# Optimization experiments

Hardware: AMD Instinct MI355X
Metric: run time of the kernel (lower is better)

## Reference

```python
import jax, jax.numpy as jnp
import numpy as np

B, L, D, H, NL = 4, 2048, 1024, 4, 2
HD = D // H
FF = 4 * D
EPS = 1e-5


def layernorm(x, g, b):
    mu = jnp.mean(x, axis=-1, keepdims=True)
    var = jnp.mean(jnp.square(x - mu), axis=-1, keepdims=True)
    return (x - mu) * jax.lax.rsqrt(var + EPS) * g + b


def setup_inputs() -> dict:
    key = jax.random.key(0)
    ks = jax.random.split(key, 8)
    std = 0.02
    return {
        "x": jax.random.normal(ks[0], (B, L, 3 * D), dtype=jnp.float32),
        "w3d": jax.random.normal(ks[1], (D, 3 * D), dtype=jnp.float32) * std,
        "b3d": jnp.zeros((D,), jnp.float32),
        "ln1_g": jnp.ones((NL, D), jnp.float32),
        "ln1_b": jnp.zeros((NL, D), jnp.float32),
        "wqkv": jax.random.normal(ks[2], (NL, 3 * D, D), dtype=jnp.float32) * std,
        "bqkv": jnp.zeros((NL, 3 * D), jnp.float32),
        "wproj": jax.random.normal(ks[3], (NL, D, D), dtype=jnp.float32) * std,
        "bproj": jnp.zeros((NL, D), jnp.float32),
        "ln2_g": jnp.ones((NL, D), jnp.float32),
        "ln2_b": jnp.zeros((NL, D), jnp.float32),
        "w1": jax.random.normal(ks[4], (NL, FF, D), dtype=jnp.float32) * std,
        "b1": jnp.zeros((NL, FF), jnp.float32),
        "w2": jax.random.normal(ks[5], (NL, D, FF), dtype=jnp.float32) * std,
        "b2": jnp.zeros((NL, D), jnp.float32),
        "lnf_g": jnp.ones((D,), jnp.float32),
        "lnf_b": jnp.zeros((D,), jnp.float32),
    }


def reference(x, w3d, b3d, ln1_g, ln1_b, wqkv, bqkv, wproj, bproj,
              ln2_g, ln2_b, w1, b1, w2, b2, lnf_g, lnf_b):
    h = jnp.einsum('bli,di->bld', x, w3d) + b3d
    scale = 1.0 / jnp.sqrt(jnp.float32(HD))
    for i in range(NL):
        # attention block
        res = h
        hn = layernorm(h, ln1_g[i], ln1_b[i])
        qkv = jnp.einsum('bld,ed->ble', hn, wqkv[i]) + bqkv[i]  # [B,L,3D]
        qkv = qkv.reshape(B, L, 3, H, HD)
        q, k, v = qkv[:, :, 0], qkv[:, :, 1], qkv[:, :, 2]  # [B,L,H,HD]
        attn = jnp.einsum('bqhd,bkhd->bhqk', q, k) * scale
        attn = jax.nn.softmax(attn, axis=-1)
        o = jnp.einsum('bhqk,bkhd->bqhd', attn, v).reshape(B, L, D)
        h = res + jnp.einsum('bld,ed->ble', o, wproj[i]) + bproj[i]
        # FFN block
        res = h
        hn = layernorm(h, ln2_g[i], ln2_b[i])
        f = jnp.einsum('bld,fd->blf', hn, w1[i]) + b1[i]
        f = jax.nn.gelu(f, approximate=False)  # torch nn.GELU default is exact
        h = res + jnp.einsum('blf,df->bld', f, w2[i]) + b2[i]
    return layernorm(h, lnf_g, lnf_b)
```

## Files before the change

### kernel.cpp

```cpp
#include <hip/hip_runtime.h>
#include <cstdint>
#include <cstddef>

#define BATCH   4
#define L_SEQ   2048
#define DMODEL  1024
#define NHEAD   4
#define HDIM    256
#define FFDIM   4096
#define MROWS   (BATCH * L_SEQ)
#define NLAYER  2

typedef __bf16 bf16_t;
typedef __bf16 bf16x8 __attribute__((ext_vector_type(8)));
typedef __bf16 bf16x4 __attribute__((ext_vector_type(4)));
typedef float  floatx4 __attribute__((ext_vector_type(4)));

__device__ __forceinline__ void async_cp16(const void* g, void* l) {
  auto gp = reinterpret_cast<__attribute__((address_space(1))) void*>(
      reinterpret_cast<uintptr_t>(g));
  auto lp = reinterpret_cast<__attribute__((address_space(3))) void*>(
      reinterpret_cast<uintptr_t>(l));
  __builtin_amdgcn_global_load_lds(gp, lp, 16, 0, 0);
}

__global__ __launch_bounds__(256)
void cvt_f32_bf16(const float* __restrict__ in, bf16_t* __restrict__ out, int n4) {
  int i = blockIdx.x * 256 + threadIdx.x;
  if (i >= n4) return;
  float4 v = ((const float4*)in)[i];
  bf16x4 ov = { (bf16_t)v.x, (bf16_t)v.y, (bf16_t)v.z, (bf16_t)v.w };
  ((bf16x4*)out)[i] = ov;
}

template<bool BF16OUT>
__global__ __launch_bounds__(256)
void ln_kernel(const float* __restrict__ x, const float* __restrict__ gw,
               const float* __restrict__ bw, void* __restrict__ outp) {
  const int row = blockIdx.x;
  const int tid = threadIdx.x;
  const float4 v = ((const float4*)(x + (size_t)row * DMODEL))[tid];
  float s  = v.x + v.y + v.z + v.w;
  float ss = v.x * v.x + v.y * v.y + v.z * v.z + v.w * v.w;
#pragma unroll
  for (int o = 32; o > 0; o >>= 1) {
    s  += __shfl_xor(s, o);
    ss += __shfl_xor(ss, o);
  }
  __shared__ float red0[4], red1[4];
  const int wv = tid >> 6;
  if ((tid & 63) == 0) { red0[wv] = s; red1[wv] = ss; }
  __syncthreads();
  s  = red0[0] + red0[1] + red0[2] + red0[3];
  ss = red1[0] + red1[1] + red1[2] + red1[3];
  const float mu  = s * (1.0f / DMODEL);
  const float var = ss * (1.0f / DMODEL) - mu * mu;
  const float rs  = rsqrtf(var + 1e-5f);
  const float4 g4 = ((const float4*)gw)[tid];
  const float4 b4 = ((const float4*)bw)[tid];
  const float o0 = (v.x - mu) * rs * g4.x + b4.x;
  const float o1 = (v.y - mu) * rs * g4.y + b4.y;
  const float o2 = (v.z - mu) * rs * g4.z + b4.z;
  const float o3 = (v.w - mu) * rs * g4.w + b4.w;
  if (BF16OUT) {
    bf16x4 ov = { (bf16_t)o0, (bf16_t)o1, (bf16_t)o2, (bf16_t)o3 };
    ((bf16x4*)outp)[(size_t)row * (DMODEL / 4) + tid] = ov;
  } else {
    float4 ov = { o0, o1, o2, o3 };
    ((float4*)outp)[(size_t)row * (DMODEL / 4) + tid] = ov;
  }
}

__global__ __launch_bounds__(256)
void softmax_kernel(bf16_t* __restrict__ S) {
  const size_t row = blockIdx.x;
  bf16_t* p = S + row * (size_t)L_SEQ + (size_t)threadIdx.x * 8;
  bf16x8 rv = *(const bf16x8*)p;
  float v[8];
  float mx = -1e30f;
#pragma unroll
  for (int j = 0; j < 8; ++j) { v[j] = (float)rv[j]; mx = fmaxf(mx, v[j]); }
#pragma unroll
  for (int o = 32; o > 0; o >>= 1) mx = fmaxf(mx, __shfl_xor(mx, o));
  __shared__ float sm[4], ssum[4];
  const int lane = threadIdx.x & 63, wv = threadIdx.x >> 6;
  if (lane == 0) sm[wv] = mx;
  __syncthreads();
  mx = fmaxf(fmaxf(sm[0], sm[1]), fmaxf(sm[2], sm[3]));
  float sum = 0.0f;
#pragma unroll
  for (int j = 0; j < 8; ++j) { v[j] = __expf(v[j] - mx); sum += v[j]; }
#pragma unroll
  for (int o = 32; o > 0; o >>= 1) sum += __shfl_xor(sum, o);
  if (lane == 0) ssum[wv] = sum;
  __syncthreads();
  sum = ssum[0] + ssum[1] + ssum[2] + ssum[3];
  const float inv = 1.0f / sum;
  bf16x8 ov;
#pragma unroll
  for (int j = 0; j < 8; ++j) ov[j] = (bf16_t)(v[j] * inv);
  *(bf16x8*)p = ov;
}

__global__ __launch_bounds__(256)
void transpose_v(const bf16_t* __restrict__ vt, bf16_t* __restrict__ vT) {
  __shared__ bf16_t tile[64][65];
  const int z = blockIdx.z, b = z >> 2, head = z & 3;
  const int l0 = blockIdx.x * 64, hd0 = blockIdx.y * 64;
  const int x = threadIdx.x & 63, y4 = threadIdx.x >> 6;
#pragma unroll
  for (int r = 0; r < 64; r += 4) {
    const int l = l0 + y4 + r;
    tile[y4 + r][x] =
        vt[((size_t)b * L_SEQ + l) * DMODEL + head * HDIM + hd0 + x];
  }
  __syncthreads();
#pragma unroll
  for (int r = 0; r < 64; r += 4) {
    const int hd = hd0 + y4 + r;
    vT[((size_t)z * HDIM + hd) * L_SEQ + l0 + x] = tile[x][y4 + r];
  }
}

struct EpiBiasF32 {
  float* C; const float* bias; int ldc;
  __device__ __forceinline__ void store(int, int m, int n, float v) const {
    C[(size_t)m * ldc + n] = v + bias[n];
  }
};
struct EpiResBiasF32 {
  float* C; const float* bias; int ldc;
  __device__ __forceinline__ void store(int, int m, int n, float v) const {
    const size_t idx = (size_t)m * ldc + n;
    C[idx] = C[idx] + v + bias[n];
  }
};
struct EpiGeluBf16 {
  bf16_t* C; const float* bias; int ldc;
  __device__ __forceinline__ void store(int, int m, int n, float v) const {
    const float t = v + bias[n];
    const float g = 0.5f * t * (1.0f + erff(t * 0.7071067811865475f));
    C[(size_t)m * ldc + n] = (bf16_t)g;
  }
};
struct EpiQKV {
  bf16_t *q, *k, *vt; const float* bias;
  __device__ __forceinline__ void store(int, int m, int n, float v) const {
    const float t = v + bias[n];
    const int b = m >> 11, l = m & 2047;
    const int which = n >> 10, e = n & 1023;
    const int head = e >> 8, hd = e & 255;
    const bf16_t x = (bf16_t)t;
    if (which == 0)
      q[(((size_t)(b * NHEAD + head)) * L_SEQ + l) * HDIM + hd] = x;
    else if (which == 1)
      k[(((size_t)(b * NHEAD + head)) * L_SEQ + l) * HDIM + hd] = x;
    else
      vt[(size_t)m * DMODEL + e] = x;
  }
};
struct EpiScaleBf16 {
  bf16_t* C; long strideC; int ldc; float scale;
  __device__ __forceinline__ void store(int z, int m, int n, float v) const {
    C[(size_t)z * strideC + (size_t)m * ldc + n] = (bf16_t)(v * scale);
  }
};
struct EpiOBf16 {
  bf16_t* C;
  __device__ __forceinline__ void store(int z, int m, int n, float v) const {
    C[((size_t)(z >> 2) * L_SEQ + m) * DMODEL + (z & 3) * HDIM + n] = (bf16_t)v;
  }
};

template<class Epi>
__global__ __launch_bounds__(256, 3)
void gemm_bt(const bf16_t* __restrict__ A, int lda, long strideA,
             const bf16_t* __restrict__ B, int ldb, long strideB,
             int K, Epi epi) {
  __shared__ bf16_t lsA[128 * 64];
  __shared__ bf16_t lsB[128 * 64];
  const int tid  = threadIdx.x;
  const int wave = tid >> 6, lane = tid & 63;
  const int z = blockIdx.z;
  A += (size_t)z * strideA;
  B += (size_t)z * strideB;
  const int m0 = blockIdx.y * 128, n0 = blockIdx.x * 128;

  const int rl = lane >> 3, p = lane & 7;
  const int csw = (p ^ rl) * 8;
  const int rbase = wave * 32 + rl;
  const bf16_t* gA = A + (size_t)(m0 + rbase) * lda + csw;
  const bf16_t* gB = B + (size_t)(n0 + rbase) * ldb + csw;
  bf16_t* lA = &lsA[wave * 32 * 64];
  bf16_t* lB = &lsB[wave * 32 * 64];

  const int wm = wave >> 1, wn = wave & 1;
  const int lane15 = lane & 15, quad = lane >> 4;
  const int arow = wm * 64 + lane15;
  const int brow = wn * 64 + lane15;
  const int sw = lane15 & 7;
  const int koff0 = ((quad + 0) ^ sw) * 8;
  const int koff1 = ((quad + 4) ^ sw) * 8;

  floatx4 acc[4][4] = {};

  for (int k0 = 0; k0 < K; k0 += 64) {
#pragma unroll
    for (int j = 0; j < 4; ++j) {
      async_cp16(gA + k0 + (size_t)j * 8 * lda, lA + j * 8 * 64);
      async_cp16(gB + k0 + (size_t)j * 8 * ldb, lB + j * 8 * 64);
    }
    __syncthreads();
#pragma unroll
    for (int kk = 0; kk < 2; ++kk) {
      const int ko = kk ? koff1 : koff0;
      bf16x8 af[4], bfr[4];
#pragma unroll
      for (int i = 0; i < 4; ++i)
        af[i] = *(const bf16x8*)&lsA[(arow + i * 16) * 64 + ko];
#pragma unroll
      for (int j = 0; j < 4; ++j)
        bfr[j] = *(const bf16x8*)&lsB[(brow + j * 16) * 64 + ko];
#pragma unroll
      for (int i = 0; i < 4; ++i)
#pragma unroll
        for (int j = 0; j < 4; ++j)
          acc[i][j] = __builtin_amdgcn_mfma_f32_16x16x32_bf16(af[i], bfr[j],
                                                              acc[i][j], 0, 0, 0);
    }
    __syncthreads();
  }

#pragma unroll
  for (int i = 0; i < 4; ++i) {
    const int mbase = m0 + wm * 64 + i * 16 + quad * 4;
#pragma unroll
    for (int j = 0; j < 4; ++j) {
      const int nloc = n0 + wn * 64 + j * 16 + lane15;
#pragma unroll
      for (int r = 0; r < 4; ++r)
        epi.store(z, mbase + r, nloc, acc[i][j][r]);
    }
  }
}

extern "C" void kernel_launch(void* const* d_in, const int* in_sizes, int n_in,
                              void* d_out, int out_size, void* d_ws, size_t ws_size,
                              hipStream_t stream) {
  const float* x_in  = (const float*)d_in[0];
  const float* w3d   = (const float*)d_in[1];
  const float* b3d   = (const float*)d_in[2];
  const float* ln1g  = (const float*)d_in[3];
  const float* ln1b  = (const float*)d_in[4];
  const float* wqkv  = (const float*)d_in[5];
  const float* bqkv  = (const float*)d_in[6];
  const float* wproj = (const float*)d_in[7];
  const float* bproj = (const float*)d_in[8];
  const float* ln2g  = (const float*)d_in[9];
  const float* ln2b  = (const float*)d_in[10];
  const float* w1    = (const float*)d_in[11];
  const float* b1    = (const float*)d_in[12];
  const float* w2    = (const float*)d_in[13];
  const float* b2    = (const float*)d_in[14];
  const float* lnfg  = (const float*)d_in[15];
  const float* lnfb  = (const float*)d_in[16];
  float* out = (float*)d_out;

  char* ws = (char*)d_ws;
  size_t off = 0;
  auto alloc = [&](size_t bytes) -> void* {
    void* p = ws + off;
    off = (off + bytes + 255) & ~(size_t)255;
    return p;
  };
  float*  h      = (float*) alloc((size_t)MROWS * DMODEL * 4);
  bf16_t* hn     = (bf16_t*)alloc((size_t)MROWS * DMODEL * 2);
  bf16_t* w3db   = (bf16_t*)alloc((size_t)DMODEL * 3 * DMODEL * 2);
  bf16_t* wqkvb  = (bf16_t*)alloc((size_t)NLAYER * 3 * DMODEL * DMODEL * 2);
  bf16_t* wprojb = (bf16_t*)alloc((size_t)NLAYER * DMODEL * DMODEL * 2);
  bf16_t* w1b    = (bf16_t*)alloc((size_t)NLAYER * FFDIM * DMODEL * 2);
  bf16_t* w2b    = (bf16_t*)alloc((size_t)NLAYER * DMODEL * FFDIM * 2);
  char*   r1     = (char*)  alloc(3ull * 16777216);
  bf16_t* xb     = (bf16_t*)r1;
  bf16_t* qb     = (bf16_t*)r1;
  bf16_t* kb     = (bf16_t*)(r1 + 16777216);
  bf16_t* vtmp   = (bf16_t*)(r1 + 2ull * 16777216);
  bf16_t* vT     = (bf16_t*)alloc(16777216);
  bf16_t* ob     = (bf16_t*)alloc(16777216);
  char*   r2     = (char*)  alloc(134217728);
  bf16_t* S      = (bf16_t*)r2;
  bf16_t* f      = (bf16_t*)r2;
  (void)ws_size; (void)in_sizes; (void)n_in; (void)out_size;

  auto cvt = [&](const float* src, bf16_t* dst, size_t n) {
    int n4 = (int)(n / 4);
    cvt_f32_bf16<<<(n4 + 255) / 256, 256, 0, stream>>>(src, dst, n4);
  };
  cvt(x_in,  xb,     (size_t)MROWS * 3 * DMODEL);
  cvt(w3d,   w3db,   (size_t)DMODEL * 3 * DMODEL);
  cvt(wqkv,  wqkvb,  (size_t)NLAYER * 3 * DMODEL * DMODEL);
  cvt(wproj, wprojb, (size_t)NLAYER * DMODEL * DMODEL);
  cvt(w1,    w1b,    (size_t)NLAYER * FFDIM * DMODEL);
  cvt(w2,    w2b,    (size_t)NLAYER * DMODEL * FFDIM);

  gemm_bt<<<dim3(DMODEL / 128, MROWS / 128, 1), 256, 0, stream>>>(
      xb, 3 * DMODEL, 0L, w3db, 3 * DMODEL, 0L, 3 * DMODEL,
      EpiBiasF32{h, b3d, DMODEL});

  for (int i = 0; i < NLAYER; ++i) {
    ln_kernel<true><<<MROWS, 256, 0, stream>>>(h, ln1g + i * DMODEL,
                                               ln1b + i * DMODEL, hn);
    gemm_bt<<<dim3(3 * DMODEL / 128, MROWS / 128, 1), 256, 0, stream>>>(
        hn, DMODEL, 0L, wqkvb + (size_t)i * 3 * DMODEL * DMODEL, DMODEL, 0L,
        DMODEL, EpiQKV{qb, kb, vtmp, bqkv + i * 3 * DMODEL});
    transpose_v<<<dim3(L_SEQ / 64, HDIM / 64, BATCH * NHEAD), 256, 0, stream>>>(
        vtmp, vT);
    gemm_bt<<<dim3(L_SEQ / 128, L_SEQ / 128, BATCH * NHEAD), 256, 0, stream>>>(
        qb, HDIM, (long)L_SEQ * HDIM, kb, HDIM, (long)L_SEQ * HDIM, HDIM,
        EpiScaleBf16{S, (long)L_SEQ * L_SEQ, L_SEQ, 0.0625f});
    softmax_kernel<<<BATCH * NHEAD * L_SEQ, 256, 0, stream>>>(S);
    gemm_bt<<<dim3(HDIM / 128, L_SEQ / 128, BATCH * NHEAD), 256, 0, stream>>>(
        S, L_SEQ, (long)L_SEQ * L_SEQ, vT, L_SEQ, (long)HDIM * L_SEQ, L_SEQ,
        EpiOBf16{ob});
    gemm_bt<<<dim3(DMODEL / 128, MROWS / 128, 1), 256, 0, stream>>>(
        ob, DMODEL, 0L, wprojb + (size_t)i * DMODEL * DMODEL, DMODEL, 0L,
        DMODEL, EpiResBiasF32{h, bproj + i * DMODEL, DMODEL});
    ln_kernel<true><<<MROWS, 256, 0, stream>>>(h, ln2g + i * DMODEL,
                                               ln2b + i * DMODEL, hn);
    gemm_bt<<<dim3(FFDIM / 128, MROWS / 128, 1), 256, 0, stream>>>(
        hn, DMODEL, 0L, w1b + (size_t)i * FFDIM * DMODEL, DMODEL, 0L, DMODEL,
        EpiGeluBf16{f, b1 + i * FFDIM, FFDIM});
    gemm_bt<<<dim3(DMODEL / 128, MROWS / 128, 1), 256, 0, stream>>>(
        f, FFDIM, 0L, w2b + (size_t)i * DMODEL * FFDIM, FFDIM, 0L, FFDIM,
        EpiResBiasF32{h, b2 + i * DMODEL, DMODEL});
  }

  ln_kernel<false><<<MROWS, 256, 0, stream>>>(h, lnfg, lnfb, out);
}
```

Before: 1.323 ms.

## Replace materialized attention with fused flash-attention kernel and direct V-transpose epilogue

```diff
diff --git a/kernel.cpp b/kernel.cpp
--- a/kernel.cpp
+++ b/kernel.cpp
@@ -71,104 +71,176 @@
   }
 }
 
-__global__ __launch_bounds__(256)
-void softmax_kernel(bf16_t* __restrict__ S) {
-  const size_t row = blockIdx.x;
-  bf16_t* p = S + row * (size_t)L_SEQ + (size_t)threadIdx.x * 8;
-  bf16x8 rv = *(const bf16x8*)p;
-  float v[8];
-  float mx = -1e30f;
-#pragma unroll
-  for (int j = 0; j < 8; ++j) { v[j] = (float)rv[j]; mx = fmaxf(mx, v[j]); }
-#pragma unroll
-  for (int o = 32; o > 0; o >>= 1) mx = fmaxf(mx, __shfl_xor(mx, o));
-  __shared__ float sm[4], ssum[4];
-  const int lane = threadIdx.x & 63, wv = threadIdx.x >> 6;
-  if (lane == 0) sm[wv] = mx;
-  __syncthreads();
-  mx = fmaxf(fmaxf(sm[0], sm[1]), fmaxf(sm[2], sm[3]));
-  float sum = 0.0f;
-#pragma unroll
-  for (int j = 0; j < 8; ++j) { v[j] = __expf(v[j] - mx); sum += v[j]; }
-#pragma unroll
-  for (int o = 32; o > 0; o >>= 1) sum += __shfl_xor(sum, o);
-  if (lane == 0) ssum[wv] = sum;
-  __syncthreads();
-  sum = ssum[0] + ssum[1] + ssum[2] + ssum[3];
-  const float inv = 1.0f / sum;
-  bf16x8 ov;
-#pragma unroll
-  for (int j = 0; j < 8; ++j) ov[j] = (bf16_t)(v[j] * inv);
-  *(bf16x8*)p = ov;
-}
-
-__global__ __launch_bounds__(256)
-void transpose_v(const bf16_t* __restrict__ vt, bf16_t* __restrict__ vT) {
-  __shared__ bf16_t tile[64][65];
-  const int z = blockIdx.z, b = z >> 2, head = z & 3;
-  const int l0 = blockIdx.x * 64, hd0 = blockIdx.y * 64;
-  const int x = threadIdx.x & 63, y4 = threadIdx.x >> 6;
-#pragma unroll
-  for (int r = 0; r < 64; r += 4) {
-    const int l = l0 + y4 + r;
-    tile[y4 + r][x] =
-        vt[((size_t)b * L_SEQ + l) * DMODEL + head * HDIM + hd0 + x];
-  }
-  __syncthreads();
-#pragma unroll
-  for (int r = 0; r < 64; r += 4) {
-    const int hd = hd0 + y4 + r;
-    vT[((size_t)z * HDIM + hd) * L_SEQ + l0 + x] = tile[x][y4 + r];
+__global__ __launch_bounds__(512, 2)
+void flash_attn(const bf16_t* __restrict__ Q, const bf16_t* __restrict__ K,
+                const bf16_t* __restrict__ VT, bf16_t* __restrict__ O) {
+  __shared__ bf16_t lsK[64 * 256];
+  __shared__ bf16_t lsV[256 * 64];
+  const int tid = threadIdx.x, wave = tid >> 6, lane = tid & 63;
+  const int lane15 = lane & 15, quad = lane >> 4;
+  const int z = blockIdx.y, qt = blockIdx.x;
+  const bf16_t* Qz = Q + (size_t)z * L_SEQ * HDIM;
+  const bf16_t* Kz = K + (size_t)z * L_SEQ * HDIM;
+  const bf16_t* Vz = VT + (size_t)z * HDIM * L_SEQ;
+
+  const int qrow = qt * 128 + wave * 16 + lane15;
+  bf16x8 qf[8];
+#pragma unroll
+  for (int kc = 0; kc < 8; ++kc)
+    qf[kc] = *(const bf16x8*)(Qz + (size_t)qrow * HDIM + kc * 32 + quad * 8);
+
+  floatx4 oacc[16] = {};
+  float m_run = -1e30f, l_run = 0.f;
+
+  const int krl = lane >> 5, kp = lane & 31;
+  const int vrl = lane >> 3, vp = lane & 7;
+  bf16_t* Pw = lsK + wave * 1024;
+
+  for (int kt = 0; kt < L_SEQ; kt += 64) {
+#pragma unroll
+    for (int j = 0; j < 4; ++j) {
+      const int i = wave * 4 + j;
+      const int r = 2 * i + krl;
+      const int col = ((kp & 24) | ((kp ^ r) & 7)) * 8;
+      async_cp16(Kz + (size_t)(kt + r) * HDIM + col, lsK + i * 512);
+      const int rv = 8 * i + vrl;
+      const int colv = ((vp ^ rv) & 7) * 8;
+      async_cp16(Vz + (size_t)rv * L_SEQ + kt + colv, lsV + i * 512);
+    }
+    __syncthreads();
+
+    floatx4 sacc[4] = {};
+#pragma unroll
+    for (int kc = 0; kc < 8; ++kc) {
+#pragma unroll
+      for (int mf = 0; mf < 4; ++mf) {
+        const int rr = mf * 16 + lane15;
+        const int c = kc * 4 + quad;
+        const int phys = (c & 24) | ((c ^ rr) & 7);
+        bf16x8 af = *(const bf16x8*)(lsK + rr * 256 + phys * 8);
+        sacc[mf] = __builtin_amdgcn_mfma_f32_16x16x32_bf16(af, qf[kc],
+                                                           sacc[mf], 0, 0, 0);
+      }
+    }
+
+    float p[4][4];
+    float mx = -1e30f;
+#pragma unroll
+    for (int mf = 0; mf < 4; ++mf)
+#pragma unroll
+      for (int r = 0; r < 4; ++r) {
+        p[mf][r] = sacc[mf][r] * 0.0625f;
+        mx = fmaxf(mx, p[mf][r]);
+      }
+    mx = fmaxf(mx, __shfl_xor(mx, 16));
+    mx = fmaxf(mx, __shfl_xor(mx, 32));
+    const float m_new = fmaxf(m_run, mx);
+    const float alpha = __expf(m_run - m_new);
+    float rs = 0.f;
+#pragma unroll
+    for (int mf = 0; mf < 4; ++mf)
+#pragma unroll
+      for (int r = 0; r < 4; ++r) {
+        p[mf][r] = __expf(p[mf][r] - m_new);
+        rs += p[mf][r];
+      }
+    rs += __shfl_xor(rs, 16);
+    rs += __shfl_xor(rs, 32);
+    l_run = l_run * alpha + rs;
+    m_run = m_new;
+#pragma unroll
+    for (int mf = 0; mf < 16; ++mf)
+#pragma unroll
+      for (int r = 0; r < 4; ++r) oacc[mf][r] *= alpha;
+
+    __syncthreads();
+
+#pragma unroll
+    for (int mf = 0; mf < 4; ++mf) {
+      bf16x4 pk = { (bf16_t)p[mf][0], (bf16_t)p[mf][1],
+                    (bf16_t)p[mf][2], (bf16_t)p[mf][3] };
+      const int c = mf * 2 + (quad >> 1);
+      const int phys = c ^ (lane15 & 7);
+      *(bf16x4*)(Pw + lane15 * 64 + phys * 8 + (quad & 1) * 4) = pk;
+    }
+
+#pragma unroll
+    for (int kc = 0; kc < 2; ++kc) {
+      const int cb = kc * 4 + quad;
+      const int pb = cb ^ (lane15 & 7);
+      bf16x8 bfr = *(const bf16x8*)(Pw + lane15 * 64 + pb * 8);
+#pragma unroll
+      for (int mf = 0; mf < 16; ++mf) {
+        const int rr = mf * 16 + lane15;
+        const int phys = cb ^ (rr & 7);
+        bf16x8 af = *(const bf16x8*)(lsV + rr * 64 + phys * 8);
+        oacc[mf] = __builtin_amdgcn_mfma_f32_16x16x32_bf16(af, bfr,
+                                                           oacc[mf], 0, 0, 0);
+      }
+    }
+    __syncthreads();
+  }
+
+  const float inv = 1.0f / l_run;
+  const int b = z >> 2, head = z & 3;
+  bf16_t* orow = O + ((size_t)b * L_SEQ + qrow) * DMODEL + head * HDIM;
+#pragma unroll
+  for (int mf = 0; mf < 16; ++mf) {
+    const int hd = mf * 16 + quad * 4;
+    bf16x4 ov = { (bf16_t)(oacc[mf][0] * inv), (bf16_t)(oacc[mf][1] * inv),
+                  (bf16_t)(oacc[mf][2] * inv), (bf16_t)(oacc[mf][3] * inv) };
+    *(bf16x4*)(orow + hd) = ov;
   }
 }
 
 struct EpiBiasF32 {
   float* C; const float* bias; int ldc;
-  __device__ __forceinline__ void store(int, int m, int n, float v) const {
-    C[(size_t)m * ldc + n] = v + bias[n];
+  __device__ __forceinline__ void store4(int, int m, int n, floatx4 v) const {
+    const float bb = bias[n];
+#pragma unroll
+    for (int r = 0; r < 4; ++r) C[(size_t)(m + r) * ldc + n] = v[r] + bb;
   }
 };
 struct EpiResBiasF32 {
   float* C; const float* bias; int ldc;
-  __device__ __forceinline__ void store(int, int m, int n, float v) const {
-    const size_t idx = (size_t)m * ldc + n;
-    C[idx] = C[idx] + v + bias[n];
+  __device__ __forceinline__ void store4(int, int m, int n, floatx4 v) const {
+    const float bb = bias[n];
+#pragma unroll
+    for (int r = 0; r < 4; ++r) {
+      const size_t idx = (size_t)(m + r) * ldc + n;
+      C[idx] = C[idx] + v[r] + bb;
+    }
   }
 };
 struct EpiGeluBf16 {
   bf16_t* C; const float* bias; int ldc;
-  __device__ __forceinline__ void store(int, int m, int n, float v) const {
-    const float t = v + bias[n];
-    const float g = 0.5f * t * (1.0f + erff(t * 0.7071067811865475f));
-    C[(size_t)m * ldc + n] = (bf16_t)g;
+  __device__ __forceinline__ void store4(int, int m, int n, floatx4 v) const {
+    const float bb = bias[n];
+#pragma unroll
+    for (int r = 0; r < 4; ++r) {
+      const float t = v[r] + bb;
+      const float g = 0.5f * t * (1.0f + erff(t * 0.7071067811865475f));
+      C[(size_t)(m + r) * ldc + n] = (bf16_t)g;
+    }
   }
 };
 struct EpiQKV {
-  bf16_t *q, *k, *vt; const float* bias;
-  __device__ __forceinline__ void store(int, int m, int n, float v) const {
-    const float t = v + bias[n];
+  bf16_t *q, *k, *vT; const float* bias;
+  __device__ __forceinline__ void store4(int, int m, int n, floatx4 v) const {
+    const float bb = bias[n];
     const int b = m >> 11, l = m & 2047;
     const int which = n >> 10, e = n & 1023;
     const int head = e >> 8, hd = e & 255;
-    const bf16_t x = (bf16_t)t;
-    if (which == 0)
-      q[(((size_t)(b * NHEAD + head)) * L_SEQ + l) * HDIM + hd] = x;
-    else if (which == 1)
-      k[(((size_t)(b * NHEAD + head)) * L_SEQ + l) * HDIM + hd] = x;
-    else
-      vt[(size_t)m * DMODEL + e] = x;
-  }
-};
-struct EpiScaleBf16 {
-  bf16_t* C; long strideC; int ldc; float scale;
-  __device__ __forceinline__ void store(int z, int m, int n, float v) const {
-    C[(size_t)z * strideC + (size_t)m * ldc + n] = (bf16_t)(v * scale);
-  }
-};
-struct EpiOBf16 {
-  bf16_t* C;
-  __device__ __forceinline__ void store(int z, int m, int n, float v) const {
-    C[((size_t)(z >> 2) * L_SEQ + m) * DMODEL + (z & 3) * HDIM + n] = (bf16_t)v;
+    const int z = b * NHEAD + head;
+    if (which == 2) {
+      bf16x4 ov = { (bf16_t)(v[0] + bb), (bf16_t)(v[1] + bb),
+                    (bf16_t)(v[2] + bb), (bf16_t)(v[3] + bb) };
+      *(bf16x4*)(vT + ((size_t)z * HDIM + hd) * L_SEQ + l) = ov;
+    } else {
+      bf16_t* dst = (which == 0 ? q : k) + ((size_t)z * L_SEQ + l) * HDIM + hd;
+#pragma unroll
+      for (int r = 0; r < 4; ++r) dst[(size_t)r * HDIM] = (bf16_t)(v[r] + bb);
+    }
   }
 };
 
@@ -237,9 +309,7 @@
 #pragma unroll
     for (int j = 0; j < 4; ++j) {
       const int nloc = n0 + wn * 64 + j * 16 + lane15;
-#pragma unroll
-      for (int r = 0; r < 4; ++r)
-        epi.store(z, mbase + r, nloc, acc[i][j][r]);
+      epi.store4(z, mbase, nloc, acc[i][j]);
     }
   }
 }
@@ -280,16 +350,12 @@
   bf16_t* wprojb = (bf16_t*)alloc((size_t)NLAYER * DMODEL * DMODEL * 2);
   bf16_t* w1b    = (bf16_t*)alloc((size_t)NLAYER * FFDIM * DMODEL * 2);
   bf16_t* w2b    = (bf16_t*)alloc((size_t)NLAYER * DMODEL * FFDIM * 2);
-  char*   r1     = (char*)  alloc(3ull * 16777216);
-  bf16_t* xb     = (bf16_t*)r1;
-  bf16_t* qb     = (bf16_t*)r1;
-  bf16_t* kb     = (bf16_t*)(r1 + 16777216);
-  bf16_t* vtmp   = (bf16_t*)(r1 + 2ull * 16777216);
-  bf16_t* vT     = (bf16_t*)alloc(16777216);
-  bf16_t* ob     = (bf16_t*)alloc(16777216);
-  char*   r2     = (char*)  alloc(134217728);
-  bf16_t* S      = (bf16_t*)r2;
-  bf16_t* f      = (bf16_t*)r2;
+  bf16_t* xb     = (bf16_t*)alloc((size_t)MROWS * 3 * DMODEL * 2);
+  bf16_t* qb     = (bf16_t*)alloc((size_t)MROWS * DMODEL * 2);
+  bf16_t* kb     = (bf16_t*)alloc((size_t)MROWS * DMODEL * 2);
+  bf16_t* vT     = (bf16_t*)alloc((size_t)MROWS * DMODEL * 2);
+  bf16_t* ob     = (bf16_t*)alloc((size_t)MROWS * DMODEL * 2);
+  bf16_t* f      = (bf16_t*)alloc((size_t)MROWS * FFDIM * 2);
   (void)ws_size; (void)in_sizes; (void)n_in; (void)out_size;
 
   auto cvt = [&](const float* src, bf16_t* dst, size_t n) {
@@ -312,16 +378,9 @@
                                                ln1b + i * DMODEL, hn);
     gemm_bt<<<dim3(3 * DMODEL / 128, MROWS / 128, 1), 256, 0, stream>>>(
         hn, DMODEL, 0L, wqkvb + (size_t)i * 3 * DMODEL * DMODEL, DMODEL, 0L,
-        DMODEL, EpiQKV{qb, kb, vtmp, bqkv + i * 3 * DMODEL});
-    transpose_v<<<dim3(L_SEQ / 64, HDIM / 64, BATCH * NHEAD), 256, 0, stream>>>(
-        vtmp, vT);
-    gemm_bt<<<dim3(L_SEQ / 128, L_SEQ / 128, BATCH * NHEAD), 256, 0, stream>>>(
-        qb, HDIM, (long)L_SEQ * HDIM, kb, HDIM, (long)L_SEQ * HDIM, HDIM,
-        EpiScaleBf16{S, (long)L_SEQ * L_SEQ, L_SEQ, 0.0625f});
-    softmax_kernel<<<BATCH * NHEAD * L_SEQ, 256, 0, stream>>>(S);
-    gemm_bt<<<dim3(HDIM / 128, L_SEQ / 128, BATCH * NHEAD), 256, 0, stream>>>(
-        S, L_SEQ, (long)L_SEQ * L_SEQ, vT, L_SEQ, (long)HDIM * L_SEQ, L_SEQ,
-        EpiOBf16{ob});
+        DMODEL, EpiQKV{qb, kb, vT, bqkv + i * 3 * DMODEL});
+    flash_attn<<<dim3(L_SEQ / 128, BATCH * NHEAD), 512, 0, stream>>>(
+        qb, kb, vT, ob);
     gemm_bt<<<dim3(DMODEL / 128, MROWS / 128, 1), 256, 0, stream>>>(
         ob, DMODEL, 0L, wprojb + (size_t)i * DMODEL * DMODEL, DMODEL, 0L,
         DMODEL, EpiResBiasF32{h, bproj + i * DMODEL, DMODEL});
```

Measured after the change: 1.281 ms. 1.03x faster.
